# Optimization experiments

Hardware: AMD Instinct MI355X
Metric: run time of the kernel (lower is better)

The kernel has to match this reference:

```python
import jax, jax.numpy as jnp
import numpy as np

D_MODEL = 1024

def setup_inputs() -> dict:
    key = jax.random.key(0)
    ks = jax.random.split(key, 7)
    x = jax.random.normal(ks[0], (4, 4096, D_MODEL), dtype=jnp.float32)
    s = 1.0 / np.sqrt(D_MODEL)
    Wq = jax.random.uniform(ks[1], (D_MODEL, D_MODEL), jnp.float32, -s, s)
    bq = jax.random.uniform(ks[2], (D_MODEL,), jnp.float32, -s, s)
    Wk = jax.random.uniform(ks[3], (D_MODEL, D_MODEL), jnp.float32, -s, s)
    bk = jax.random.uniform(ks[4], (D_MODEL,), jnp.float32, -s, s)
    Wv = jax.random.uniform(ks[5], (D_MODEL, D_MODEL), jnp.float32, -s, s)
    bv = jax.random.uniform(ks[6], (D_MODEL,), jnp.float32, -s, s)
    return {"x": x, "Wq": Wq, "bq": bq, "Wk": Wk, "bk": bk, "Wv": Wv, "bv": bv}

def reference(x, Wq, bq, Wk, bk, Wv, bv):
    # Q, K, V: [b, s, d]
    Q = jnp.einsum('bsd,ed->bse', x, Wq) + bq
    K = jnp.einsum('bsd,ed->bse', x, Wk) + bk
    V = jnp.einsum('bsd,ed->bse', x, Wv) + bv
    scale = 1.0 / jnp.sqrt(jnp.asarray(D_MODEL, dtype=x.dtype))
    scores = jnp.einsum('bqd,bkd->bqk', Q, K) * scale  # [b, s, s]
    attn = jax.nn.softmax(scores, axis=-1)
    return jnp.einsum('bqk,bkd->bqd', attn, V)
```

## Files before the change

kernel.cpp:

```cpp
#include <hip/hip_runtime.h>
#include <stdint.h>
#include <stddef.h>

#define DM 1024
#define SEQ 4096
#define NB 4
#define NTOK (NB*SEQ)

typedef __attribute__((ext_vector_type(8))) short s16x8;
typedef __attribute__((ext_vector_type(4))) float f32x4;

__device__ __forceinline__ unsigned short f2bf(float f) {
  unsigned int u = __float_as_uint(f);
  u += 0x7FFFu + ((u >> 16) & 1u);
  return (unsigned short)(u >> 16);
}
__device__ __forceinline__ float bf2f(unsigned short u) {
  return __uint_as_float((unsigned int)u << 16);
}

__device__ __forceinline__ f32x4 mfma16(s16x8 a, s16x8 b, f32x4 c) {
  return __builtin_amdgcn_mfma_f32_16x16x32_bf16(a, b, c, 0, 0, 0);
}

__device__ __forceinline__ void gload16(const void* g, void* l) {
  __builtin_amdgcn_global_load_lds((const __attribute__((address_space(1))) unsigned int*)g,
                                   (__attribute__((address_space(3))) unsigned int*)l, 16, 0, 0);
}

__device__ __forceinline__ void xcd_swz(int gx, int gy, int& x, int& y, int& z) {
  int nwg = gx * gy * gridDim.z;
  int bid = blockIdx.x + gx * (blockIdx.y + gy * blockIdx.z);
  int cpx = nwg >> 3;
  int wg = (bid & 7) * cpx + (bid >> 3);
  x = wg % gx; int t = wg / gx; y = t % gy; z = t / gy;
}

__global__ void k_conv4(const float* __restrict__ x, const float* __restrict__ wq,
                        const float* __restrict__ wk, const float* __restrict__ wv,
                        unsigned short* __restrict__ xb, unsigned short* __restrict__ wb) {
  const int n0 = NTOK * DM / 8;
  const int n1 = DM * DM / 8;
  int i0 = blockIdx.x * blockDim.x + threadIdx.x;
  int st = gridDim.x * blockDim.x;
  for (int i = i0; i < n0 + 3 * n1; i += st) {
    const float* s; unsigned short* d; int k;
    if (i < n0) { s = x; d = xb; k = i; }
    else {
      int j = i - n0; int seg = j >> 17; k = j & (n1 - 1);
      s = (seg == 0) ? wq : (seg == 1) ? wk : wv;
      d = wb + (size_t)seg * DM * DM;
    }
    const f32x4* sp = (const f32x4*)s + (size_t)k * 2;
    f32x4 a = sp[0], b = sp[1];
    s16x8 o;
    o[0] = (short)f2bf(a[0]); o[1] = (short)f2bf(a[1]);
    o[2] = (short)f2bf(a[2]); o[3] = (short)f2bf(a[3]);
    o[4] = (short)f2bf(b[0]); o[5] = (short)f2bf(b[1]);
    o[6] = (short)f2bf(b[2]); o[7] = (short)f2bf(b[3]);
    *((s16x8*)d + k) = o;
  }
}

template<int KD, int BK, int EPI>
__device__ __forceinline__ void gemm_core(
    unsigned short (*lds)[2][128 * BK],
    const unsigned short* __restrict__ A, const unsigned short* __restrict__ B,
    void* __restrict__ outp, int ldc, const float* __restrict__ aux, float scale,
    int mbase, int nbase)
{
  constexpr int NT     = KD / BK;
  constexpr int SLOTS  = BK / 8;
  constexpr int SMASK  = SLOTS - 1;
  constexpr int PASSES = 128 * SLOTS / 256;

  const int tid = threadIdx.x, lane = tid & 63, wid = tid >> 6;
  const int wr = wid >> 1, wc = wid & 1;
  const int l15 = lane & 15, lg = lane >> 4;

  f32x4 acc[4][4];
  #pragma unroll
  for (int m = 0; m < 4; m++)
    #pragma unroll
    for (int n = 0; n < 4; n++) { acc[m][n][0]=0.f; acc[m][n][1]=0.f; acc[m][n][2]=0.f; acc[m][n][3]=0.f; }

  auto rswz = [](int row) -> int { return (BK == 64) ? (row & 7) : ((row >> 1) & 3); };

  auto stage = [&](int buf, int kt) {
    const int kb_ = kt * BK;
    #pragma unroll
    for (int p = 0; p < PASSES; p++) {
      int s = p * 256 + tid;
      int row = s / SLOTS, sl = (s & SMASK) ^ rswz(row);
      gload16(A + (size_t)(mbase + row) * KD + kb_ + sl * 8, &lds[buf][0][s * 8]);
    }
    #pragma unroll
    for (int p = 0; p < PASSES; p++) {
      int s = p * 256 + tid;
      int row = s / SLOTS, sl = (s & SMASK) ^ rswz(row);
      gload16(B + (size_t)(nbase + row) * KD + kb_ + sl * 8, &lds[buf][1][s * 8]);
    }
  };

  auto compute = [&](int buf) {
    #pragma unroll
    for (int k2 = 0; k2 < BK / 32; k2++) {
      s16x8 af[4], bf[4];
      #pragma unroll
      for (int m = 0; m < 4; m++) {
        int row = wr * 64 + m * 16 + l15;
        int sl = (k2 * 4 + lg) ^ rswz(row);
        af[m] = *(const s16x8*)(&lds[buf][0][0] + row * BK + sl * 8);
      }
      #pragma unroll
      for (int n = 0; n < 4; n++) {
        int row = wc * 64 + n * 16 + l15;
        int sl = (k2 * 4 + lg) ^ rswz(row);
        bf[n] = *(const s16x8*)(&lds[buf][1][0] + row * BK + sl * 8);
      }
      #pragma unroll
      for (int m = 0; m < 4; m++)
        #pragma unroll
        for (int n = 0; n < 4; n++)
          acc[m][n] = mfma16(af[m], bf[n], acc[m][n]);
    }
  };

  stage(0, 0);
  __syncthreads();
  for (int kt = 0; kt < NT; kt++) {
    int cur = kt & 1;
    if (kt < NT - 1) stage(cur ^ 1, kt + 1);
    compute(cur);
    __syncthreads();
  }

  #pragma unroll
  for (int n = 0; n < 4; n++) {
    int col = nbase + wc * 64 + n * 16 + l15;
    float cb = (EPI == 0) ? aux[col] : 0.f;
    #pragma unroll
    for (int m = 0; m < 4; m++) {
      #pragma unroll
      for (int r = 0; r < 4; r++) {
        int row = mbase + wr * 64 + m * 16 + lg * 4 + r;
        float v = acc[m][n][r];
        if (EPI == 0) {
          ((unsigned short*)outp)[(size_t)row * ldc + col] = f2bf(v + cb);
        } else if (EPI == 1) {
          ((unsigned short*)outp)[(size_t)row * ldc + col] = f2bf(__expf(v * scale));
        } else if (EPI == 3) {
          ((unsigned short*)outp)[(size_t)row * ldc + col] = f2bf(v + aux[row]);
        } else {
          ((float*)outp)[(size_t)row * ldc + col] = v * aux[row];
        }
      }
    }
  }
}

__global__ __launch_bounds__(256, 4) void k_qkv(
    const unsigned short* __restrict__ xb, const unsigned short* __restrict__ wb,
    const float* __restrict__ b0, const float* __restrict__ b1, const float* __restrict__ bv,
    unsigned short* __restrict__ qo, unsigned short* __restrict__ ko, unsigned short* __restrict__ vt)
{
  __shared__ unsigned short lds[2][2][128 * 32];
  int x, y, z;
  xcd_swz(8, 128, x, y, z);
  if (z < 2) {
    gemm_core<DM, 32, 0>(lds, xb, wb + (size_t)z * DM * DM,
                         z ? ko : qo, DM, z ? b1 : b0, 0.f,
                         y * 128, x * 128);
  } else {
    int batch = y >> 5, tokb = (y & 31) * 128;
    gemm_core<DM, 32, 3>(lds, wb + (size_t)2 * DM * DM, xb + (size_t)batch * SEQ * DM,
                         vt + (size_t)batch * DM * SEQ, SEQ, bv, 0.f,
                         x * 128, tokb);
  }
}

__global__ __launch_bounds__(256, 4) void k_sgemm(
    const unsigned short* __restrict__ qb, const unsigned short* __restrict__ kb,
    unsigned short* __restrict__ s0, unsigned short* __restrict__ s1,
    unsigned short* __restrict__ s2, unsigned short* __restrict__ s3, int bb)
{
  __shared__ unsigned short lds[2][2][128 * 32];
  int bid = blockIdx.x + 32 * (blockIdx.y + 32 * blockIdx.z);
  int xcd = bid & 7, wg = bid >> 3;
  int x, y, z;
  if (gridDim.z == 4) {
    z = xcd >> 1;
    int y0 = (xcd & 1) << 4;
    int xc = wg >> 7, r = wg & 127;
    x = xc * 8 + (r & 7);
    y = y0 + (r >> 3);
  } else {
    z = xcd >> 2;
    int y0 = (xcd & 3) << 3;
    int xc = wg >> 6, r = wg & 63;
    x = xc * 8 + (r & 7);
    y = y0 + (r >> 3);
  }
  unsigned short* sc = (z == 0) ? s0 : (z == 1) ? s1 : (z == 2) ? s2 : s3;
  gemm_core<DM, 32, 1>(lds, qb + (size_t)(bb + z) * SEQ * DM, kb + (size_t)(bb + z) * SEQ * DM,
                       sc, SEQ, nullptr, 0.03125f,
                       y * 128, x * 128);
}

__global__ __launch_bounds__(256) void k_rowsum(
    const unsigned short* __restrict__ s0, const unsigned short* __restrict__ s1,
    const unsigned short* __restrict__ s2, const unsigned short* __restrict__ s3,
    float* __restrict__ linv, int bb) {
  const int z = blockIdx.z;
  const unsigned short* sc = (z == 0) ? s0 : (z == 1) ? s1 : (z == 2) ? s2 : s3;
  const int row = blockIdx.x * 4 + (threadIdx.x >> 6);
  const int lane = threadIdx.x & 63;
  const unsigned short* rp = sc + (size_t)row * SEQ + lane * 8;
  float s = 0.f;
  #pragma unroll
  for (int j = 0; j < 8; j++) {
    s16x8 v = *(const s16x8*)(rp + (size_t)j * 512);
    #pragma unroll
    for (int t = 0; t < 8; t++) s += bf2f((unsigned short)v[t]);
  }
  s += __shfl_xor(s, 1);  s += __shfl_xor(s, 2);  s += __shfl_xor(s, 4);
  s += __shfl_xor(s, 8);  s += __shfl_xor(s, 16); s += __shfl_xor(s, 32);
  if (lane == 0) linv[(size_t)(bb + z) * SEQ + row] = 1.f / s;
}

__global__ __launch_bounds__(256, 2) void k_pv(
    const unsigned short* __restrict__ s0, const unsigned short* __restrict__ s1,
    const unsigned short* __restrict__ s2, const unsigned short* __restrict__ s3,
    const unsigned short* __restrict__ vt, const float* __restrict__ linv,
    float* __restrict__ out, int bb)
{
  __shared__ unsigned short lds[2][2][128 * 64];
  int x, y, z;
  xcd_swz(8, 32, x, y, z);
  const unsigned short* sc = (z == 0) ? s0 : (z == 1) ? s1 : (z == 2) ? s2 : s3;
  gemm_core<SEQ, 64, 4>(lds, sc, vt + (size_t)(bb + z) * DM * SEQ,
                        out + (size_t)(bb + z) * SEQ * DM, DM,
                        linv + (size_t)(bb + z) * SEQ, 1.f,
                        y * 128, x * 128);
}

extern "C" void kernel_launch(void* const* d_in, const int* in_sizes, int n_in,
                              void* d_out, int out_size, void* d_ws, size_t ws_size,
                              hipStream_t stream) {
  const float* x  = (const float*)d_in[0];
  const float* Wq = (const float*)d_in[1];
  const float* bq = (const float*)d_in[2];
  const float* Wk = (const float*)d_in[3];
  const float* bk = (const float*)d_in[4];
  const float* Wv = (const float*)d_in[5];
  const float* bv = (const float*)d_in[6];
  float* out = (float*)d_out;
  char* ws = (char*)d_ws;

  unsigned short* xb  = (unsigned short*)(ws);
  unsigned short* wb  = (unsigned short*)(ws + 33554432);
  unsigned short* qb  = (unsigned short*)(ws + 39845888);
  unsigned short* kb  = (unsigned short*)(ws + 73400320);
  unsigned short* sc1 = (unsigned short*)(ws + 106954752);
  unsigned short* vt  = (unsigned short*)(ws + 140509184);
  float* linv         = (float*)(ws + 174063616);
  unsigned short* sc0 = xb;
  unsigned short* sc2 = (unsigned short*)(ws + 174129152);
  unsigned short* sc3 = (unsigned short*)(ws + 207683584);
  const bool big = ws_size >= 241238016ull;

  k_conv4<<<2048, 256, 0, stream>>>(x, Wq, Wk, Wv, xb, wb);
  k_qkv<<<dim3(8, 128, 3), 256, 0, stream>>>(xb, wb, bq, bk, bv, qb, kb, vt);

  if (big) {
    k_sgemm<<<dim3(32, 32, 4), 256, 0, stream>>>(qb, kb, sc0, sc1, sc2, sc3, 0);
    k_rowsum<<<dim3(1024, 1, 4), 256, 0, stream>>>(sc0, sc1, sc2, sc3, linv, 0);
    k_pv<<<dim3(8, 32, 4), 256, 0, stream>>>(sc0, sc1, sc2, sc3, vt, linv, out, 0);
  } else {
    for (int bb = 0; bb < NB; bb += 2) {
      k_sgemm<<<dim3(32, 32, 2), 256, 0, stream>>>(qb, kb, sc0, sc1, sc0, sc1, bb);
      k_rowsum<<<dim3(1024, 1, 2), 256, 0, stream>>>(sc0, sc1, sc0, sc1, linv, bb);
      k_pv<<<dim3(8, 32, 2), 256, 0, stream>>>(sc0, sc1, sc0, sc1, vt, linv, out, bb);
    }
  }
}
```

Before: 458.6 us.

## Fuse softmax row-sum partials into score GEMM epilogue, drop rowsum pass

The score GEMM epilogue now accumulates the exponentiated values per row, reduces them across lanes with shuffles, and writes one partial sum per 64-column tile into a scratch buffer that reuses the weight workspace. A small k_psum kernel then adds up the 64 partials per row and stores the reciprocal. This replaces the k_rowsum pass, which had to re-read the whole bf16 score matrix. The PV kernel also drops its XCD swizzle and uses plain block indices, which may change L2 locality. The fallback path for a small workspace still uses k_rowsum, while its score GEMM writes partials it never reads.

```diff
diff --git a/kernel.cpp b/kernel.cpp
--- a/kernel.cpp
+++ b/kernel.cpp
@@ -67,7 +67,7 @@
     unsigned short (*lds)[2][128 * BK],
     const unsigned short* __restrict__ A, const unsigned short* __restrict__ B,
     void* __restrict__ outp, int ldc, const float* __restrict__ aux, float scale,
-    int mbase, int nbase)
+    float* __restrict__ part, int mbase, int nbase)
 {
   constexpr int NT     = KD / BK;
   constexpr int SLOTS  = BK / 8;
@@ -135,6 +135,12 @@
     __syncthreads();
   }
 
+  float rowpart[16];
+  if (EPI == 1) {
+    #pragma unroll
+    for (int i = 0; i < 16; i++) rowpart[i] = 0.f;
+  }
+
   #pragma unroll
   for (int n = 0; n < 4; n++) {
     int col = nbase + wc * 64 + n * 16 + l15;
@@ -148,12 +154,27 @@
         if (EPI == 0) {
           ((unsigned short*)outp)[(size_t)row * ldc + col] = f2bf(v + cb);
         } else if (EPI == 1) {
-          ((unsigned short*)outp)[(size_t)row * ldc + col] = f2bf(__expf(v * scale));
+          float e = __expf(v * scale);
+          ((unsigned short*)outp)[(size_t)row * ldc + col] = f2bf(e);
+          rowpart[m * 4 + r] += e;
         } else if (EPI == 3) {
           ((unsigned short*)outp)[(size_t)row * ldc + col] = f2bf(v + aux[row]);
         } else {
           ((float*)outp)[(size_t)row * ldc + col] = v * aux[row];
         }
+      }
+    }
+  }
+
+  if (EPI == 1) {
+    #pragma unroll
+    for (int i = 0; i < 16; i++) {
+      float rs = rowpart[i];
+      rs += __shfl_xor(rs, 1); rs += __shfl_xor(rs, 2);
+      rs += __shfl_xor(rs, 4); rs += __shfl_xor(rs, 8);
+      if (l15 == 0) {
+        int row = mbase + wr * 64 + (i >> 2) * 16 + lg * 4 + (i & 3);
+        part[(size_t)row * 64 + (nbase >> 6) + wc] = rs;
       }
     }
   }
@@ -169,12 +190,12 @@
   xcd_swz(8, 128, x, y, z);
   if (z < 2) {
     gemm_core<DM, 32, 0>(lds, xb, wb + (size_t)z * DM * DM,
-                         z ? ko : qo, DM, z ? b1 : b0, 0.f,
+                         z ? ko : qo, DM, z ? b1 : b0, 0.f, nullptr,
                          y * 128, x * 128);
   } else {
     int batch = y >> 5, tokb = (y & 31) * 128;
     gemm_core<DM, 32, 3>(lds, wb + (size_t)2 * DM * DM, xb + (size_t)batch * SEQ * DM,
-                         vt + (size_t)batch * DM * SEQ, SEQ, bv, 0.f,
+                         vt + (size_t)batch * DM * SEQ, SEQ, bv, 0.f, nullptr,
                          x * 128, tokb);
   }
 }
@@ -182,7 +203,8 @@
 __global__ __launch_bounds__(256, 4) void k_sgemm(
     const unsigned short* __restrict__ qb, const unsigned short* __restrict__ kb,
     unsigned short* __restrict__ s0, unsigned short* __restrict__ s1,
-    unsigned short* __restrict__ s2, unsigned short* __restrict__ s3, int bb)
+    unsigned short* __restrict__ s2, unsigned short* __restrict__ s3,
+    float* __restrict__ lpart, int bb)
 {
   __shared__ unsigned short lds[2][2][128 * 32];
   int bid = blockIdx.x + 32 * (blockIdx.y + 32 * blockIdx.z);
@@ -204,7 +226,18 @@
   unsigned short* sc = (z == 0) ? s0 : (z == 1) ? s1 : (z == 2) ? s2 : s3;
   gemm_core<DM, 32, 1>(lds, qb + (size_t)(bb + z) * SEQ * DM, kb + (size_t)(bb + z) * SEQ * DM,
                        sc, SEQ, nullptr, 0.03125f,
+                       lpart + (size_t)(bb + z) * SEQ * 64,
                        y * 128, x * 128);
+}
+
+__global__ __launch_bounds__(256) void k_psum(const float* __restrict__ part,
+                                              float* __restrict__ linv) {
+  int r = blockIdx.x * 256 + threadIdx.x;
+  const f32x4* p = (const f32x4*)(part + (size_t)r * 64);
+  float s = 0.f;
+  #pragma unroll
+  for (int j = 0; j < 16; j++) { f32x4 v = p[j]; s += v[0] + v[1] + v[2] + v[3]; }
+  linv[r] = 1.f / s;
 }
 
 __global__ __launch_bounds__(256) void k_rowsum(
@@ -235,12 +268,11 @@
     float* __restrict__ out, int bb)
 {
   __shared__ unsigned short lds[2][2][128 * 64];
-  int x, y, z;
-  xcd_swz(8, 32, x, y, z);
+  int x = blockIdx.x, y = blockIdx.y, z = blockIdx.z;
   const unsigned short* sc = (z == 0) ? s0 : (z == 1) ? s1 : (z == 2) ? s2 : s3;
   gemm_core<SEQ, 64, 4>(lds, sc, vt + (size_t)(bb + z) * DM * SEQ,
                         out + (size_t)(bb + z) * SEQ * DM, DM,
-                        linv + (size_t)(bb + z) * SEQ, 1.f,
+                        linv + (size_t)(bb + z) * SEQ, 1.f, nullptr,
                         y * 128, x * 128);
 }
 
@@ -265,6 +297,7 @@
   unsigned short* vt  = (unsigned short*)(ws + 140509184);
   float* linv         = (float*)(ws + 174063616);
   unsigned short* sc0 = xb;
+  float* lpart        = (float*)wb;
   unsigned short* sc2 = (unsigned short*)(ws + 174129152);
   unsigned short* sc3 = (unsigned short*)(ws + 207683584);
   const bool big = ws_size >= 241238016ull;
@@ -273,12 +306,12 @@
   k_qkv<<<dim3(8, 128, 3), 256, 0, stream>>>(xb, wb, bq, bk, bv, qb, kb, vt);
 
   if (big) {
-    k_sgemm<<<dim3(32, 32, 4), 256, 0, stream>>>(qb, kb, sc0, sc1, sc2, sc3, 0);
-    k_rowsum<<<dim3(1024, 1, 4), 256, 0, stream>>>(sc0, sc1, sc2, sc3, linv, 0);
+    k_sgemm<<<dim3(32, 32, 4), 256, 0, stream>>>(qb, kb, sc0, sc1, sc2, sc3, lpart, 0);
+    k_psum<<<NTOK / 256, 256, 0, stream>>>(lpart, linv);
     k_pv<<<dim3(8, 32, 4), 256, 0, stream>>>(sc0, sc1, sc2, sc3, vt, linv, out, 0);
   } else {
     for (int bb = 0; bb < NB; bb += 2) {
-      k_sgemm<<<dim3(32, 32, 2), 256, 0, stream>>>(qb, kb, sc0, sc1, sc0, sc1, bb);
+      k_sgemm<<<dim3(32, 32, 2), 256, 0, stream>>>(qb, kb, sc0, sc1, sc0, sc1, lpart, bb);
       k_rowsum<<<dim3(1024, 1, 2), 256, 0, stream>>>(sc0, sc1, sc0, sc1, linv, bb);
       k_pv<<<dim3(8, 32, 2), 256, 0, stream>>>(sc0, sc1, sc0, sc1, vt, linv, out, bb);
     }
```

New measurement: 489.6 us. 6.8% more time.
